# Kernel optimization log

Measured on AMD Instinct MI355X. Metric: run time of the kernel, lower is better.

Reference implementation:

```python
import jax, jax.numpy as jnp
import numpy as np

COST_LABELS = 2.0
COST_BBOX = 5.0
COST_GIOU = 2.0
NUM_HEADS = 7
NUM_CLASSES = 16


def setup_inputs() -> dict:
    key = jax.random.key(0)
    k0, k1, k2, k3 = jax.random.split(key, 4)
    bs, nq, nt = 16, 900, 100
    return {
        "pred_logits": jax.random.normal(k0, (NUM_HEADS, bs, nq, NUM_CLASSES), jnp.float32),
        "pred_boxes": jax.random.uniform(k1, (bs, nq, 4), jnp.float32),
        "tgt_boxes": jax.random.uniform(k2, (bs, nt, 4), jnp.float32),
        "tgt_labels": jax.random.randint(k3, (NUM_HEADS, bs, nt), 0, NUM_CLASSES),
    }


def box_cxcywh_to_xyxy(b):
    cx, cy, w, h = jnp.split(b, 4, axis=-1)
    return jnp.concatenate([cx - 0.5 * w, cy - 0.5 * h, cx + 0.5 * w, cy + 0.5 * h], axis=-1)


def generalized_box_iou(a, b):
    # a: [N,4] xyxy, b: [M,4] xyxy -> [N,M]
    area_a = (a[:, 2] - a[:, 0]) * (a[:, 3] - a[:, 1])
    area_b = (b[:, 2] - b[:, 0]) * (b[:, 3] - b[:, 1])
    lt = jnp.maximum(a[:, None, :2], b[None, :, :2])
    rb = jnp.minimum(a[:, None, 2:], b[None, :, 2:])
    wh = jnp.clip(rb - lt, 0.0)
    inter = wh[..., 0] * wh[..., 1]
    union = area_a[:, None] + area_b[None, :] - inter
    iou = inter / union
    lt_e = jnp.minimum(a[:, None, :2], b[None, :, :2])
    rb_e = jnp.maximum(a[:, None, 2:], b[None, :, 2:])
    wh_e = jnp.clip(rb_e - lt_e, 0.0)
    area = wh_e[..., 0] * wh_e[..., 1]
    return iou - (area - union) / area


@jax.jit
def compute_cost(pred_logits, pred_boxes, tgt_boxes, tgt_labels):
    bs, nq, _ = pred_boxes.shape
    out_bbox = pred_boxes.reshape(-1, 4)   # [N,4] cxcywh
    tgt_bbox = tgt_boxes.reshape(-1, 4)    # [M,4] cxcywh
    # L1 cdist
    cost_bbox = jnp.sum(jnp.abs(out_bbox[:, None, :] - tgt_bbox[None, :, :]), axis=-1)
    cost_giou = -generalized_box_iou(box_cxcywh_to_xyxy(out_bbox), box_cxcywh_to_xyxy(tgt_bbox))
    # label cost: sum over the 7 heads of -sigmoid(logits)[:, tgt_ids]
    probs = jax.nn.sigmoid(pred_logits.reshape(NUM_HEADS, -1, NUM_CLASSES))  # [7,N,C]
    ids = tgt_labels.reshape(NUM_HEADS, -1)                                   # [7,M]
    cost_labels = jnp.zeros_like(cost_bbox)
    for h in range(NUM_HEADS):  # small fixed loop, avoids a [7,N,M] intermediate
        cost_labels = cost_labels - probs[h][:, ids[h]]
    C = COST_BBOX * cost_bbox + COST_LABELS * cost_labels + COST_GIOU * cost_giou
    return C.reshape(bs, nq, -1)  # [bs, nq, bs*nt]


def _lsa(cost):
    """Jonker-Volgenant shortest augmenting path. cost: [r,c] with r<=c.
    Returns row2col: optimal column for each row (minimizes total cost)."""
    cost = np.asarray(cost, dtype=np.float64)
    r, c = cost.shape
    u = np.zeros(r + 1)
    v = np.zeros(c + 1)
    p = np.zeros(c + 1, np.int64)    # p[j] = row matched to column j (1-indexed)
    way = np.zeros(c + 1, np.int64)
    for i in range(1, r + 1):
        p[0] = i
        j0 = 0
        minv = np.full(c + 1, np.inf)
        used = np.zeros(c + 1, bool)
        while True:
            used[j0] = True
            i0 = p[j0]
            free = np.nonzero(~used)[0]  # unused columns (1..c)
            cur = cost[i0 - 1, free - 1] - u[i0] - v[free]
            better = cur < minv[free]
            minv[free] = np.where(better, cur, minv[free])
            way[free[better]] = j0
            k = np.argmin(minv[free])
            j1 = free[k]
            delta = minv[free][k]
            u[p[used]] += delta
            v[used] -= delta
            minv[free] -= delta
            j0 = j1
            if p[j0] == 0:
                break
        while j0:
            j1 = way[j0]
            p[j0] = p[j1]
            j0 = j1
    row2col = np.full(r, -1, np.int64)
    for j in range(1, c + 1):
        if p[j] > 0:
            row2col[p[j] - 1] = j - 1
    return row2col


def reference(pred_logits, pred_boxes, tgt_boxes, tgt_labels):
    C = compute_cost(pred_logits, pred_boxes, tgt_boxes, tgt_labels)  # [bs, nq, bs*nt]
    bs, nq, M = C.shape
    nt = M // bs
    Cn = np.asarray(C)
    out = np.zeros((bs, 2, nt), np.int64)
    for b in range(bs):
        sub = Cn[b, :, b * nt:(b + 1) * nt]  # [nq, nt] per-image block (mimics C.split(sizes))
        t2p = _lsa(sub.T)                    # for each target, its matched prediction
        order = np.argsort(t2p, kind="stable")  # scipy returns row indices sorted
        out[b, 0] = t2p[order]  # index_i: selected predictions (sorted)
        out[b, 1] = order       # index_j: corresponding targets
    return jnp.asarray(out)
```

## Files before the change

kernel.cpp:

```cpp
#include <hip/hip_runtime.h>
#include <hip/hip_bf16.h>
#include <math.h>

#define NQ 900
#define NT 100
#define BS 16
#define NH 7
#define NC 16
#define NSLOT 16
#define MAXTREE 8192

__global__ __launch_bounds__(256) void sig_transpose_kernel(const float* __restrict__ logits,
                                                            float* __restrict__ probsT) {
    const int hb = blockIdx.x;
    const float* src = logits + (size_t)hb * NQ * NC;
    float* dst = probsT + (size_t)hb * NC * NQ;
    __shared__ float tile[NC][NQ + 1];
    for (int e = threadIdx.x; e < NQ * NC; e += 256) {
        int q = e >> 4, c = e & 15;
        float x = src[e];
        tile[c][q] = 1.0f / (1.0f + expf(-x));
    }
    __syncthreads();
    for (int c = 0; c < NC; ++c)
        for (int q = threadIdx.x; q < NQ; q += 256)
            dst[c * NQ + q] = tile[c][q];
}

__global__ __launch_bounds__(256) void cost_kernel_bt(const float4* __restrict__ pboxes4,
                                                      const float4* __restrict__ tboxes4,
                                                      const int*    __restrict__ tlabels,
                                                      const float*  __restrict__ probsT,
                                                      float* __restrict__ costT) {
    const int bt = blockIdx.x;
    const int b = bt / NT, t = bt % NT;

    const float* prow[NH];
    #pragma unroll
    for (int h = 0; h < NH; ++h) {
        int lab = tlabels[(h * BS + b) * NT + t];
        prow[h] = probsT + (size_t)((h * BS + b) * NC + lab) * NQ;
    }

    float4 tb = tboxes4[b * NT + t];
    float tx = tb.x, ty = tb.y, tw = tb.z, th = tb.w;
    float bx0 = tx - 0.5f * tw, by0 = ty - 0.5f * th;
    float bx1 = tx + 0.5f * tw, by1 = ty + 0.5f * th;
    float areaB = (bx1 - bx0) * (by1 - by0);

    for (int q = threadIdx.x; q < NQ; q += 256) {
        float4 pb = pboxes4[b * NQ + q];
        float px = pb.x, py = pb.y, pw = pb.z, ph = pb.w;

        float cost_bbox = fabsf(px - tx) + fabsf(py - ty) + fabsf(pw - tw) + fabsf(ph - th);

        float ax0 = px - 0.5f * pw, ay0 = py - 0.5f * ph;
        float ax1 = px + 0.5f * pw, ay1 = py + 0.5f * ph;
        float areaA = (ax1 - ax0) * (ay1 - ay0);
        float ltx = fmaxf(ax0, bx0), lty = fmaxf(ay0, by0);
        float rbx = fminf(ax1, bx1), rby = fminf(ay1, by1);
        float iw = fmaxf(rbx - ltx, 0.f), ih = fmaxf(rby - lty, 0.f);
        float inter = iw * ih;
        float uni = areaA + areaB - inter;
        float iou = inter / uni;
        float ex0 = fminf(ax0, bx0), ey0 = fminf(ay0, by0);
        float ex1 = fmaxf(ax1, bx1), ey1 = fmaxf(ay1, by1);
        float ew = fmaxf(ex1 - ex0, 0.f), eh = fmaxf(ey1 - ey0, 0.f);
        float earea = ew * eh;
        float giou = iou - (earea - uni) / earea;

        float ssum = 0.f;
        #pragma unroll
        for (int h = 0; h < NH; ++h) ssum += prow[h][q];

        costT[(b * NT + t) * NQ + q] = 5.0f * cost_bbox - 2.0f * ssum - 2.0f * giou;
    }
}

__global__ void cost_kernel_fb(const float* __restrict__ logits,
                               const float* __restrict__ pboxes,
                               const float* __restrict__ tboxes,
                               const int*   __restrict__ tlabels,
                               float* __restrict__ costT) {
    int id = blockIdx.x * blockDim.x + threadIdx.x;
    if (id >= BS * NT * NQ) return;
    int q = id % NQ;
    int t = (id / NQ) % NT;
    int b = id / (NQ * NT);

    const float* pb = pboxes + (b * NQ + q) * 4;
    const float* tb = tboxes + (b * NT + t) * 4;
    float px = pb[0], py = pb[1], pw = pb[2], ph = pb[3];
    float tx = tb[0], ty = tb[1], tw = tb[2], th = tb[3];

    float cost_bbox = fabsf(px - tx) + fabsf(py - ty) + fabsf(pw - tw) + fabsf(ph - th);

    float ax0 = px - 0.5f * pw, ay0 = py - 0.5f * ph;
    float ax1 = px + 0.5f * pw, ay1 = py + 0.5f * ph;
    float bx0 = tx - 0.5f * tw, by0 = ty - 0.5f * th;
    float bx1 = tx + 0.5f * tw, by1 = ty + 0.5f * th;
    float areaA = (ax1 - ax0) * (ay1 - ay0);
    float areaB = (bx1 - bx0) * (by1 - by0);
    float ltx = fmaxf(ax0, bx0), lty = fmaxf(ay0, by0);
    float rbx = fminf(ax1, bx1), rby = fminf(ay1, by1);
    float iw = fmaxf(rbx - ltx, 0.f), ih = fmaxf(rby - lty, 0.f);
    float inter = iw * ih;
    float uni = areaA + areaB - inter;
    float iou = inter / uni;
    float ex0 = fminf(ax0, bx0), ey0 = fminf(ay0, by0);
    float ex1 = fmaxf(ax1, bx1), ey1 = fmaxf(ay1, by1);
    float ew = fmaxf(ex1 - ex0, 0.f), eh = fmaxf(ey1 - ey0, 0.f);
    float earea = ew * eh;
    float giou = iou - (earea - uni) / earea;

    float ssum = 0.f;
    #pragma unroll
    for (int h = 0; h < NH; ++h) {
        int lab = tlabels[(h * BS + b) * NT + t];
        float x = logits[((h * BS + b) * NQ + q) * NC + lab];
        ssum += 1.0f / (1.0f + expf(-x));
    }

    costT[(b * NT + t) * NQ + q] = 5.0f * cost_bbox - 2.0f * ssum - 2.0f * giou;
}

__global__ __launch_bounds__(64) void lsa_kernel(const float* __restrict__ costT,
                                                 int* __restrict__ out) {
    const int b = blockIdx.x;
    const int lane = threadIdx.x;
    const float* cost = costT + b * NT * NQ;

    __shared__ double2 pu[NQ + 1];
    __shared__ double u_s[NT + 1];
    __shared__ int way2[NSLOT][64];
    __shared__ int p_w[NQ + 1];
    __shared__ int jmin_s[NT];
    __shared__ int listA[NT];
    __shared__ int r2c[NT];
    __shared__ int cnt_s;

    for (int j = lane; j <= NQ; j += 64) {
        pu[j] = make_double2(0.0, 0.0);
        p_w[j] = 0x7fffffff;
    }
    __syncthreads();

    bool lostA = false, lostB = false;
    #pragma unroll
    for (int pass = 0; pass < 2; ++pass) {
        int r = pass * 64 + lane;
        if (r < NT) {
            const float4* row4 = (const float4*)(cost + (size_t)r * NQ);
            float m0 = INFINITY, m1f = INFINITY, m2f = INFINITY, m3f = INFINITY;
            int i0 = 0, i1 = 0, i2 = 0, i3 = 0;
            #pragma unroll 5
            for (int q4 = 0; q4 < NQ / 4; ++q4) {
                float4 cv = row4[q4];
                if (cv.x < m0)  { m0 = cv.x;  i0 = 4 * q4; }
                if (cv.y < m1f) { m1f = cv.y; i1 = 4 * q4 + 1; }
                if (cv.z < m2f) { m2f = cv.z; i2 = 4 * q4 + 2; }
                if (cv.w < m3f) { m3f = cv.w; i3 = 4 * q4 + 3; }
            }
            float mv = m0; int mj = i0;
            if (m1f < mv || (m1f == mv && i1 < mj)) { mv = m1f; mj = i1; }
            if (m2f < mv || (m2f == mv && i2 < mj)) { mv = m2f; mj = i2; }
            if (m3f < mv || (m3f == mv && i3 < mj)) { mv = m3f; mj = i3; }
            u_s[r + 1] = (double)mv;
            jmin_s[r] = mj;
            atomicMin(&p_w[mj + 1], r + 1);
        }
    }
    __syncthreads();

    {
        int rA = lane;
        int j = jmin_s[rA] + 1;
        if (p_w[j] == rA + 1) pu[j] = make_double2(u_s[rA + 1], (double)(rA + 1));
        else lostA = true;
    }
    if (lane < NT - 64) {
        int rB = 64 + lane;
        int j = jmin_s[rB] + 1;
        if (p_w[j] == rB + 1) pu[j] = make_double2(u_s[rB + 1], (double)(rB + 1));
        else lostB = true;
    }
    unsigned long long mA = __ballot(lostA);
    unsigned long long mB = __ballot(lostB);
    if (lane == 0) {
        int n = 0;
        unsigned long long m = mA;
        while (m) { int l = __ffsll((unsigned long long)m) - 1; listA[n++] = l + 1; m &= m - 1; }
        m = mB;
        while (m) { int l = __ffsll((unsigned long long)m) - 1; listA[n++] = 64 + l + 1; m &= m - 1; }
        cnt_s = n;
    }
    __syncthreads();
    const int nfree = cnt_s;

    double v[NSLOT], minv[NSLOT], ureg[NSLOT];
    int pof[NSLOT];
    #pragma unroll
    for (int k = 0; k < NSLOT; ++k) { v[k] = 0.0; ureg[k] = 0.0; pof[k] = 0; }
    const unsigned invalid = (lane <= 32) ? 0u : 0xF000u;
    double u_c0 = 0.0;

    for (int ii = 0; ii < nfree; ++ii) {
        const int i = listA[ii];
        #pragma unroll
        for (int k = 0; k < NSLOT; ++k) minv[k] = INFINITY;
        unsigned used = invalid;
        int j0 = 0;
        int i0 = i;
        double u_i0 = u_s[i];

        const float4* crow4 = (const float4*)(cost + (size_t)(i0 - 1) * NQ);
        float4 c4[4];
        #pragma unroll
        for (int kc = 0; kc < 3; ++kc) c4[kc] = crow4[lane + 64 * kc];
        c4[3] = (lane <= 32) ? crow4[lane + 192] : make_float4(0.f, 0.f, 0.f, 0.f);

        int guard = 0;
        while (guard++ < MAXTREE) {
            if (j0 != 0) {
                int idx = j0 - 1;
                if (lane == ((idx >> 2) & 63)) {
                    int slot = ((idx >> 8) << 2) | (idx & 3);
                    used |= (1u << slot);
                    #pragma unroll
                    for (int s = 0; s < NSLOT; ++s)
                        if (s == slot) { pof[s] = i0; ureg[s] = u_i0; }
                }
            } else {
                if (lane == 0) u_c0 = u_i0;
            }

            double bv = INFINITY;
            int bj = 2048;
            #pragma unroll
            for (int kc = 0; kc < 4; ++kc) {
                #pragma unroll
                for (int e = 0; e < 4; ++e) {
                    const int s = 4 * kc + e;
                    if (!((used >> s) & 1u)) {
                        float cf = (e == 0) ? c4[kc].x : (e == 1) ? c4[kc].y
                                 : (e == 2) ? c4[kc].z : c4[kc].w;
                        int j = 1 + 4 * lane + 256 * kc + e;
                        double cur = ((double)cf - u_i0) - v[s];
                        if (cur < minv[s]) { minv[s] = cur; way2[s][lane] = j0; }
                        if (minv[s] < bv) { bv = minv[s]; bj = j; }
                    }
                }
            }
            double vmin = bv;
            #pragma unroll
            for (int off = 1; off < 64; off <<= 1)
                vmin = fmin(vmin, __shfl_xor(vmin, off));
            unsigned long long tied = __ballot(bv == vmin);
            int wl = __ffsll((unsigned long long)tied) - 1;
            int jwin = __shfl(bj, wl);
            const double delta = vmin;

            double2 t = pu[jwin];
            const int i0n = (int)t.y;
            float4 c4n[4];
            if (i0n != 0) {
                const float4* nrow4 = (const float4*)(cost + (size_t)(i0n - 1) * NQ);
                #pragma unroll
                for (int kc = 0; kc < 3; ++kc) c4n[kc] = nrow4[lane + 64 * kc];
                c4n[3] = (lane <= 32) ? nrow4[lane + 192] : make_float4(0.f, 0.f, 0.f, 0.f);
            }

            #pragma unroll
            for (int s = 0; s < NSLOT; ++s) {
                minv[s] -= delta;
                if ((used >> s) & 1u) { ureg[s] += delta; v[s] -= delta; }
            }
            if (lane == 0) u_c0 += delta;

            j0 = jwin;
            if (i0n == 0) break;
            i0 = i0n;
            u_i0 = t.x;
            #pragma unroll
            for (int kc = 0; kc < 4; ++kc) c4[kc] = c4n[kc];
        }

        __syncthreads();
        #pragma unroll
        for (int s = 0; s < NSLOT; ++s) {
            if (((used >> s) & 1u) && !((invalid >> s) & 1u)) {
                int j = 1 + 4 * lane + 256 * (s >> 2) + (s & 3);
                u_s[pof[s]] = ureg[s];
                pu[j] = make_double2(ureg[s], (double)pof[s]);
            }
        }
        __syncthreads();
        if (lane == 0) {
            u_s[i] = u_c0;
            int j = j0;
            while (j) {
                int idx = j - 1;
                int ol = (idx >> 2) & 63;
                int sl = ((idx >> 8) << 2) | (idx & 3);
                int jw = way2[sl][ol];
                double2 t2 = (jw == 0) ? make_double2(u_c0, (double)i) : pu[jw];
                pu[j] = t2;
                j = jw;
            }
        }
        __syncthreads();
    }

    for (int j = 1 + lane; j <= NQ; j += 64) {
        int pi = (int)pu[j].y;
        if (pi > 0) r2c[pi - 1] = j - 1;
    }
    __syncthreads();
    for (int t = lane; t < NT; t += 64) {
        int ccol = r2c[t];
        int rank = 0;
        for (int tt = 0; tt < NT; ++tt) rank += (r2c[tt] < ccol) ? 1 : 0;
        out[b * 2 * NT + rank] = ccol;
        out[b * 2 * NT + NT + rank] = t;
    }
}

extern "C" void kernel_launch(void* const* d_in, const int* in_sizes, int n_in,
                              void* d_out, int out_size, void* d_ws, size_t ws_size,
                              hipStream_t stream) {
    const float* logits  = (const float*)d_in[0];
    const float* pboxes  = (const float*)d_in[1];
    const float* tboxes  = (const float*)d_in[2];
    const int*   tlabels = (const int*)d_in[3];
    int* out = (int*)d_out;
    float* costT = (float*)d_ws;

    const size_t costT_elems  = (size_t)BS * NT * NQ;
    const size_t probsT_elems = (size_t)NH * BS * NC * NQ;
    const size_t need = (costT_elems + probsT_elems) * sizeof(float);

    if (ws_size >= need) {
        float* probsT = costT + costT_elems;
        sig_transpose_kernel<<<NH * BS, 256, 0, stream>>>(logits, probsT);
        cost_kernel_bt<<<BS * NT, 256, 0, stream>>>((const float4*)pboxes,
                                                    (const float4*)tboxes, tlabels, probsT, costT);
    } else {
        const int total = BS * NT * NQ;
        cost_kernel_fb<<<(total + 255) / 256, 256, 0, stream>>>(logits, pboxes, tboxes, tlabels, costT);
    }
    lsa_kernel<<<BS, 64, 0, stream>>>(costT, out);
}
```

Baseline: 121.3 us.

## Use lazy dual updates and register-resident column assignments in LSA kernel

Reworks the shortest-augmenting-path loop so each visited column records the distance at which it was reached. Dual potentials are then corrected once at the end of each augmentation, instead of subtracting delta from every slot on every step. The per-column row assignment and its dual now live in registers per lane and are fetched by shuffle from the winning lane, replacing a shared-memory double2 array lookup. The row prefetch of the next cost row is dropped; rows are loaded at the top of each step, which removes overlap of that global load with the reduction. Registers are refreshed from shared memory after each augmentation.

New measurement: 121.6 us. No clear change (+0.2%).

```diff
diff --git a/kernel.cpp b/kernel.cpp
--- a/kernel.cpp
+++ b/kernel.cpp
@@ -130,8 +130,8 @@
     const int lane = threadIdx.x;
     const float* cost = costT + b * NT * NQ;
 
-    __shared__ double2 pu[NQ + 1];
     __shared__ double u_s[NT + 1];
+    __shared__ int p_s[NQ + 1];
     __shared__ int way2[NSLOT][64];
     __shared__ int p_w[NQ + 1];
     __shared__ int jmin_s[NT];
@@ -140,7 +140,7 @@
     __shared__ int cnt_s;
 
     for (int j = lane; j <= NQ; j += 64) {
-        pu[j] = make_double2(0.0, 0.0);
+        p_s[j] = 0;
         p_w[j] = 0x7fffffff;
     }
     __syncthreads();
@@ -175,13 +175,13 @@
     {
         int rA = lane;
         int j = jmin_s[rA] + 1;
-        if (p_w[j] == rA + 1) pu[j] = make_double2(u_s[rA + 1], (double)(rA + 1));
+        if (p_w[j] == rA + 1) p_s[j] = rA + 1;
         else lostA = true;
     }
     if (lane < NT - 64) {
         int rB = 64 + lane;
         int j = jmin_s[rB] + 1;
-        if (p_w[j] == rB + 1) pu[j] = make_double2(u_s[rB + 1], (double)(rB + 1));
+        if (p_w[j] == rB + 1) p_s[j] = rB + 1;
         else lostB = true;
     }
     unsigned long long mA = __ballot(lostA);
@@ -197,29 +197,35 @@
     __syncthreads();
     const int nfree = cnt_s;
 
-    double v[NSLOT], minv[NSLOT], ureg[NSLOT];
-    int pof[NSLOT];
+    double v[NSLOT], minv[NSLOT], upreg[NSLOT], dreg[NSLOT];
+    int preg[NSLOT];
+    const unsigned invalid = (lane <= 32) ? 0u : 0xF000u;
     #pragma unroll
-    for (int k = 0; k < NSLOT; ++k) { v[k] = 0.0; ureg[k] = 0.0; pof[k] = 0; }
-    const unsigned invalid = (lane <= 32) ? 0u : 0xF000u;
-    double u_c0 = 0.0;
+    for (int s = 0; s < NSLOT; ++s) {
+        v[s] = 0.0; dreg[s] = 0.0;
+        int pr = 0;
+        if (!((invalid >> s) & 1u)) {
+            int j = 1 + 4 * lane + 256 * (s >> 2) + (s & 3);
+            pr = p_s[j];
+        }
+        preg[s] = pr;
+        upreg[s] = (pr > 0) ? u_s[pr] : 0.0;
+    }
+    __syncthreads();
 
     for (int ii = 0; ii < nfree; ++ii) {
         const int i = listA[ii];
         #pragma unroll
-        for (int k = 0; k < NSLOT; ++k) minv[k] = INFINITY;
+        for (int s = 0; s < NSLOT; ++s) minv[s] = INFINITY;
         unsigned used = invalid;
         int j0 = 0;
         int i0 = i;
         double u_i0 = u_s[i];
-
-        const float4* crow4 = (const float4*)(cost + (size_t)(i0 - 1) * NQ);
-        float4 c4[4];
-        #pragma unroll
-        for (int kc = 0; kc < 3; ++kc) c4[kc] = crow4[lane + 64 * kc];
-        c4[3] = (lane <= 32) ? crow4[lane + 192] : make_float4(0.f, 0.f, 0.f, 0.f);
-
+        const double u_root = u_i0;
+        double d0 = 0.0;
+        double deltaf = 0.0;
         int guard = 0;
+
         while (guard++ < MAXTREE) {
             if (j0 != 0) {
                 int idx = j0 - 1;
@@ -228,14 +234,19 @@
                     used |= (1u << slot);
                     #pragma unroll
                     for (int s = 0; s < NSLOT; ++s)
-                        if (s == slot) { pof[s] = i0; ureg[s] = u_i0; }
+                        if (s == slot) dreg[s] = d0;
                 }
-            } else {
-                if (lane == 0) u_c0 = u_i0;
-            }
-
+            }
+
+            const float4* crow4 = (const float4*)(cost + (size_t)(i0 - 1) * NQ);
+            float4 c4[4];
+            #pragma unroll
+            for (int kc = 0; kc < 3; ++kc) c4[kc] = crow4[lane + 64 * kc];
+            c4[3] = (lane <= 32) ? crow4[lane + 192] : make_float4(0.f, 0.f, 0.f, 0.f);
+
+            const double duv = d0 - u_i0;
             double bv = INFINITY;
-            int bj = 2048;
+            int bj = 2048, bs = 0;
             #pragma unroll
             for (int kc = 0; kc < 4; ++kc) {
                 #pragma unroll
@@ -244,10 +255,10 @@
                     if (!((used >> s) & 1u)) {
                         float cf = (e == 0) ? c4[kc].x : (e == 1) ? c4[kc].y
                                  : (e == 2) ? c4[kc].z : c4[kc].w;
+                        double cand = ((double)cf + duv) - v[s];
                         int j = 1 + 4 * lane + 256 * kc + e;
-                        double cur = ((double)cf - u_i0) - v[s];
-                        if (cur < minv[s]) { minv[s] = cur; way2[s][lane] = j0; }
-                        if (minv[s] < bv) { bv = minv[s]; bj = j; }
+                        if (cand < minv[s]) { minv[s] = cand; way2[s][lane] = j0; }
+                        if (minv[s] < bv) { bv = minv[s]; bj = j; bs = s; }
                     }
                 }
             }
@@ -258,61 +269,59 @@
             unsigned long long tied = __ballot(bv == vmin);
             int wl = __ffsll((unsigned long long)tied) - 1;
             int jwin = __shfl(bj, wl);
-            const double delta = vmin;
-
-            double2 t = pu[jwin];
-            const int i0n = (int)t.y;
-            float4 c4n[4];
-            if (i0n != 0) {
-                const float4* nrow4 = (const float4*)(cost + (size_t)(i0n - 1) * NQ);
-                #pragma unroll
-                for (int kc = 0; kc < 3; ++kc) c4n[kc] = nrow4[lane + 64 * kc];
-                c4n[3] = (lane <= 32) ? nrow4[lane + 192] : make_float4(0.f, 0.f, 0.f, 0.f);
-            }
-
+
+            int pb = 0; double ub = 0.0;
             #pragma unroll
-            for (int s = 0; s < NSLOT; ++s) {
-                minv[s] -= delta;
-                if ((used >> s) & 1u) { ureg[s] += delta; v[s] -= delta; }
-            }
-            if (lane == 0) u_c0 += delta;
+            for (int s = 0; s < NSLOT; ++s)
+                if (s == bs) { pb = preg[s]; ub = upreg[s]; }
+            int i0n = __shfl(pb, wl);
+            double u_n = __shfl(ub, wl);
 
             j0 = jwin;
-            if (i0n == 0) break;
+            d0 = vmin;
+            if (i0n == 0) { deltaf = vmin; break; }
             i0 = i0n;
-            u_i0 = t.x;
-            #pragma unroll
-            for (int kc = 0; kc < 4; ++kc) c4[kc] = c4n[kc];
+            u_i0 = u_n;
         }
 
         __syncthreads();
         #pragma unroll
         for (int s = 0; s < NSLOT; ++s) {
             if (((used >> s) & 1u) && !((invalid >> s) & 1u)) {
-                int j = 1 + 4 * lane + 256 * (s >> 2) + (s & 3);
-                u_s[pof[s]] = ureg[s];
-                pu[j] = make_double2(ureg[s], (double)pof[s]);
-            }
-        }
+                v[s] += (dreg[s] - deltaf);
+                u_s[preg[s]] = upreg[s] + (deltaf - dreg[s]);
+            }
+        }
+        if (lane == 0) u_s[i] = u_root + deltaf;
         __syncthreads();
         if (lane == 0) {
-            u_s[i] = u_c0;
             int j = j0;
             while (j) {
                 int idx = j - 1;
                 int ol = (idx >> 2) & 63;
                 int sl = ((idx >> 8) << 2) | (idx & 3);
                 int jw = way2[sl][ol];
-                double2 t2 = (jw == 0) ? make_double2(u_c0, (double)i) : pu[jw];
-                pu[j] = t2;
+                p_s[j] = (jw == 0) ? i : p_s[jw];
                 j = jw;
             }
         }
         __syncthreads();
-    }
-
+        #pragma unroll
+        for (int s = 0; s < NSLOT; ++s) {
+            if (!((invalid >> s) & 1u)) {
+                int j = 1 + 4 * lane + 256 * (s >> 2) + (s & 3);
+                if (((used >> s) & 1u) || (j == j0)) {
+                    int pr = p_s[j];
+                    preg[s] = pr;
+                    upreg[s] = (pr > 0) ? u_s[pr] : 0.0;
+                }
+            }
+        }
+    }
+
+    __syncthreads();
     for (int j = 1 + lane; j <= NQ; j += 64) {
-        int pi = (int)pu[j].y;
+        int pi = p_s[j];
         if (pi > 0) r2c[pi - 1] = j - 1;
     }
     __syncthreads();
```
